# Optimization experiments

Hardware: AMD Instinct MI355X
Metric: run time of the kernel (lower is better)

Reference implementation:

```python
import jax, jax.numpy as jnp
import numpy as np

MARGIN = 0.3
NUM_CLASSES = 1000


def setup_inputs() -> dict:
    key = jax.random.key(0)
    k1, k2 = jax.random.split(key)
    B, D = 8192, 256
    inputs = jax.random.normal(k1, (B, D), dtype=jnp.float32)
    targets = jax.random.randint(k2, (B,), 0, NUM_CLASSES, dtype=jnp.int64)
    return {"inputs": inputs, "targets": targets}


def reference(inputs, targets):
    # Squared Euclidean pairwise distances: ||x_i||^2 + ||x_j||^2 - 2 x_i.x_j
    sq = jnp.sum(inputs * inputs, axis=1)                      # [B]
    dist = sq[:, None] + sq[None, :] - 2.0 * (inputs @ inputs.T)  # [B, B]

    # Hard mining: per-row max over positives (same label, incl. self),
    # min over negatives, exactly as the torch per-row masked max/min loop.
    pos_mask = targets[:, None] == targets[None, :]            # [B, B] bool
    neg_inf = jnp.float32(-jnp.inf)
    pos_inf = jnp.float32(jnp.inf)
    dist_ap = jnp.max(jnp.where(pos_mask, dist, neg_inf), axis=1)  # [B]
    dist_an = jnp.min(jnp.where(pos_mask, pos_inf, dist), axis=1)  # [B]

    # MarginRankingLoss(margin)(dist_an, dist_ap, y=1) = mean relu(ap - an + m)
    loss = jnp.mean(jax.nn.relu(dist_ap - dist_an + MARGIN))
    prec = jnp.mean((dist_an > dist_ap).astype(jnp.float32))
    return (loss, prec)
```

## Files before the change

### kernel.cpp

```cpp
#include <hip/hip_runtime.h>
#include <hip/hip_bf16.h>

#define B_N 8192
#define D_K 256
#define MARGIN 0.3f

typedef float f32x4 __attribute__((ext_vector_type(4)));
typedef short s16x8 __attribute__((ext_vector_type(8)));

__device__ __forceinline__ unsigned fkey(float f) {
    unsigned u = __float_as_uint(f);
    return (u & 0x80000000u) ? ~u : (u | 0x80000000u);
}
__device__ __forceinline__ float kval(unsigned k) {
    return (k & 0x80000000u) ? __uint_as_float(k ^ 0x80000000u)
                             : __uint_as_float(~k);
}

__device__ __forceinline__ void load_lds16(const unsigned short* g,
                                           unsigned short* l) {
    __builtin_amdgcn_global_load_lds(
        (const __attribute__((address_space(1))) unsigned int*)g,
        (__attribute__((address_space(3))) unsigned int*)l, 16, 0, 0);
}

__global__ __launch_bounds__(256) void prep_kernel(const float* __restrict__ X,
        float* __restrict__ sq, unsigned* __restrict__ apk,
        unsigned* __restrict__ ank, unsigned short* __restrict__ Xp,
        float* __restrict__ acc2) {
    int row  = (blockIdx.x << 2) + (threadIdx.x >> 6);
    int lane = threadIdx.x & 63;
    const float4 v = reinterpret_cast<const float4*>(X + (size_t)row * D_K)[lane];

    float xs[4] = {v.x, v.y, v.z, v.w};
    ushort4 hv;
    unsigned short* hp = &hv.x;
    float s = 0.f;
    #pragma unroll
    for (int i = 0; i < 4; ++i) {
        __hip_bfloat16 h = __float2bfloat16(xs[i]);
        hp[i] = *reinterpret_cast<unsigned short*>(&h);
        float hf = __bfloat162float(h);
        s = fmaf(hf, hf, s);
    }
    *reinterpret_cast<ushort4*>(Xp + (size_t)row * D_K + lane * 4) = hv;

    #pragma unroll
    for (int o = 32; o > 0; o >>= 1) s += __shfl_down(s, o, 64);
    if (lane == 0) {
        sq[row]  = s;
        apk[row] = 0u;
        ank[row] = 0xFFFFFFFFu;
    }
    if (blockIdx.x == 0 && threadIdx.x == 0) {
        acc2[0] = 0.f; acc2[1] = 0.f;
        reinterpret_cast<unsigned*>(acc2)[2] = 0u;
    }
}

#define BM 128
#define BN 128

__global__ __launch_bounds__(256, 2) void dist_kernel(
        const unsigned short* __restrict__ Xp,
        const int* __restrict__ tgt, const float* __restrict__ sq,
        unsigned* __restrict__ apk, unsigned* __restrict__ ank) {
    __shared__ unsigned short Atile[2][128 * 64];
    __shared__ unsigned short Btile[2][128 * 64];

    const int t    = threadIdx.x;
    const int lane = t & 63;
    const int wave = t >> 6;
    const int wrow = (wave >> 1) * 64;
    const int wcol = (wave & 1) * 64;
    const int fr   = lane & 15;
    const int quad = lane >> 4;
    const float INF = __int_as_float(0x7f800000);

    int tt = blockIdx.x;
    int bx = (int)((sqrtf(8.f * (float)tt + 1.f) - 1.f) * 0.5f);
    while ((bx + 1) * (bx + 2) / 2 <= tt) ++bx;
    while (bx * (bx + 1) / 2 > tt) --bx;
    int by = tt - bx * (bx + 1) / 2;
    const int bm = by * BM;
    const int bn = bx * BN;

    int ct[4]; float csq[4];
    #pragma unroll
    for (int ni = 0; ni < 4; ++ni) {
        int c = bn + wcol + ni * 16 + fr;
        ct[ni] = tgt[c]; csq[ni] = sq[c];
    }
    int rt[16]; float rsq[16];
    #pragma unroll
    for (int mi = 0; mi < 4; ++mi)
        #pragma unroll
        for (int reg = 0; reg < 4; ++reg) {
            int r = bm + wrow + mi * 16 + quad * 4 + reg;
            rt[mi * 4 + reg]  = tgt[r];
            rsq[mi * 4 + reg] = sq[r];
        }

    const unsigned short* ag[4];
    const unsigned short* bg[4];
    int loff[4];
    #pragma unroll
    for (int j = 0; j < 4; ++j) {
        int g = wave * 64 + j * 256 + lane;
        int r = g >> 3, s0 = g & 7;
        int u = s0 ^ (r & 7);
        ag[j] = Xp + (size_t)(bm + r) * D_K + u * 8;
        bg[j] = Xp + (size_t)(bn + r) * D_K + u * 8;
        loff[j] = g * 8;
    }

    int aoff[4][2], boff[4][2];
    #pragma unroll
    for (int mi = 0; mi < 4; ++mi)
        #pragma unroll
        for (int h = 0; h < 2; ++h) {
            int s = (h * 4 + quad) ^ (fr & 7);
            aoff[mi][h] = (wrow + mi * 16 + fr) * 64 + s * 8;
            boff[mi][h] = (wcol + mi * 16 + fr) * 64 + s * 8;
        }

    #pragma unroll
    for (int j = 0; j < 4; ++j) {
        load_lds16(ag[j], &Atile[0][loff[j]]);
        load_lds16(bg[j], &Btile[0][loff[j]]);
    }

    f32x4 acc[4][4];
    #pragma unroll
    for (int i = 0; i < 4; ++i)
        #pragma unroll
        for (int j = 0; j < 4; ++j) acc[i][j] = (f32x4){0.f, 0.f, 0.f, 0.f};

    __syncthreads();

    #pragma unroll
    for (int win = 0; win < 4; ++win) {
        const int cur = win & 1;
        if (win < 3) {
            const int wo = (win + 1) * 64;
            #pragma unroll
            for (int j = 0; j < 4; ++j) {
                load_lds16(ag[j] + wo, &Atile[cur ^ 1][loff[j]]);
                load_lds16(bg[j] + wo, &Btile[cur ^ 1][loff[j]]);
            }
        }
        s16x8 a[4][2], b[4][2];
        #pragma unroll
        for (int mi = 0; mi < 4; ++mi)
            #pragma unroll
            for (int h = 0; h < 2; ++h) {
                a[mi][h] = *reinterpret_cast<const s16x8*>(&Atile[cur][aoff[mi][h]]);
                b[mi][h] = *reinterpret_cast<const s16x8*>(&Btile[cur][boff[mi][h]]);
            }
        __builtin_amdgcn_s_setprio(1);
        #pragma unroll
        for (int mi = 0; mi < 4; ++mi)
            #pragma unroll
            for (int ni = 0; ni < 4; ++ni) {
                acc[mi][ni] = __builtin_amdgcn_mfma_f32_16x16x32_bf16(
                    a[mi][0], b[ni][0], acc[mi][ni], 0, 0, 0);
                acc[mi][ni] = __builtin_amdgcn_mfma_f32_16x16x32_bf16(
                    a[mi][1], b[ni][1], acc[mi][ni], 0, 0, 0);
            }
        __builtin_amdgcn_s_setprio(0);
        if (win < 3) __syncthreads();
    }

    float cap[4], can[4];
    #pragma unroll
    for (int ni = 0; ni < 4; ++ni) { cap[ni] = -INF; can[ni] = INF; }

    #pragma unroll
    for (int mi = 0; mi < 4; ++mi) {
        #pragma unroll
        for (int reg = 0; reg < 4; ++reg) {
            int rl = wrow + mi * 16 + quad * 4 + reg;
            int   rti  = rt[mi * 4 + reg];
            float rsqi = rsq[mi * 4 + reg];
            float rap = -INF, ran = INF;
            #pragma unroll
            for (int ni = 0; ni < 4; ++ni) {
                float d = rsqi + csq[ni] - 2.f * acc[mi][ni][reg];
                bool pos = (rti == ct[ni]);
                if (pos) { rap = fmaxf(rap, d); cap[ni] = fmaxf(cap[ni], d); }
                else     { ran = fminf(ran, d); can[ni] = fminf(can[ni], d); }
            }
            #pragma unroll
            for (int o = 1; o < 16; o <<= 1) {
                rap = fmaxf(rap, __shfl_xor(rap, o, 64));
                ran = fminf(ran, __shfl_xor(ran, o, 64));
            }
            if (fr == 0) {
                atomicMax(&apk[bm + rl], fkey(rap));
                atomicMin(&ank[bm + rl], fkey(ran));
            }
        }
    }
    #pragma unroll
    for (int ni = 0; ni < 4; ++ni) {
        #pragma unroll
        for (int o = 16; o < 64; o <<= 1) {
            cap[ni] = fmaxf(cap[ni], __shfl_xor(cap[ni], o, 64));
            can[ni] = fminf(can[ni], __shfl_xor(can[ni], o, 64));
        }
    }
    if (lane < 16) {
        #pragma unroll
        for (int ni = 0; ni < 4; ++ni) {
            int c = bn + wcol + ni * 16 + lane;
            atomicMax(&apk[c], fkey(cap[ni]));
            atomicMin(&ank[c], fkey(can[ni]));
        }
    }
}

__global__ __launch_bounds__(256) void final_kernel(const unsigned* __restrict__ apk,
        const unsigned* __restrict__ ank, float* __restrict__ acc2,
        float* __restrict__ out) {
    __shared__ float s_sum[4], s_cnt[4];
    int i = blockIdx.x * 256 + threadIdx.x;
    float ap = kval(apk[i]);
    float an = kval(ank[i]);
    float v  = ap - an + MARGIN;
    float sum = v > 0.f ? v : 0.f;
    float cnt = an > ap ? 1.f : 0.f;
    #pragma unroll
    for (int o = 32; o > 0; o >>= 1) {
        sum += __shfl_down(sum, o, 64);
        cnt += __shfl_down(cnt, o, 64);
    }
    int wave = threadIdx.x >> 6, lane = threadIdx.x & 63;
    if (lane == 0) { s_sum[wave] = sum; s_cnt[wave] = cnt; }
    __syncthreads();
    if (threadIdx.x == 0) {
        float ts = 0.f, tc = 0.f;
        #pragma unroll
        for (int w = 0; w < 4; ++w) { ts += s_sum[w]; tc += s_cnt[w]; }
        atomicAdd(&acc2[0], ts);
        atomicAdd(&acc2[1], tc);
        __threadfence();
        unsigned ticket = atomicAdd(reinterpret_cast<unsigned*>(acc2) + 2, 1u);
        if (ticket == gridDim.x - 1) {
            float fs = atomicAdd(&acc2[0], 0.f);
            float fc = atomicAdd(&acc2[1], 0.f);
            out[0] = fs / (float)B_N;
            out[1] = fc / (float)B_N;
        }
    }
}

extern "C" void kernel_launch(void* const* d_in, const int* in_sizes, int n_in,
                              void* d_out, int out_size, void* d_ws, size_t ws_size,
                              hipStream_t stream) {
    const float* X   = (const float*)d_in[0];
    const int*   tgt = (const int*)d_in[1];

    char* ws = (char*)d_ws;
    float*          sq   = (float*)ws;
    unsigned*       apk  = (unsigned*)(ws + 32768);
    unsigned*       ank  = (unsigned*)(ws + 65536);
    float*          acc2 = (float*)(ws + 98304);
    unsigned short* Xp   = (unsigned short*)(ws + 131072);

    float* out = (float*)d_out;

    prep_kernel<<<B_N / 4, 256, 0, stream>>>(X, sq, apk, ank, Xp, acc2);
    dist_kernel<<<(64 * 65) / 2, 256, 0, stream>>>(Xp, tgt, sq, apk, ank);
    final_kernel<<<B_N / 256, 256, 0, stream>>>(apk, ank, acc2, out);
}
```

Baseline: 126.6 us.

## Enlarge distance tiles to 256x256 with 512-thread blocks and streamed B fragments

Doubles the symmetric distance tile to 256x256 using 8 waves per block, each computing a 64x128 sub-tile, so fewer tiles and less redundant global-to-LDS traffic per output. B fragments are now loaded from LDS inside the ni loop rather than all preloaded. The row/column label and norm loads are deferred until after the GEMM, and the window loop is kept rolled to reduce register pressure. LDS per block doubles to 128KB and each thread holds 128 accumulator floats, which may cut occupancy to one block per CU. The larger tiles also leave a grid of only 528 blocks, which risks poor load balance across CUs.

```diff
diff --git a/kernel.cpp b/kernel.cpp
--- a/kernel.cpp
+++ b/kernel.cpp
@@ -58,21 +58,23 @@
     }
 }
 
-#define BM 128
-#define BN 128
-
-__global__ __launch_bounds__(256, 2) void dist_kernel(
+#define BM 256
+#define BN 256
+#define NPAN (B_N / BM)
+#define NTILE (NPAN * (NPAN + 1) / 2)
+
+__global__ __launch_bounds__(512, 2) void dist_kernel(
         const unsigned short* __restrict__ Xp,
         const int* __restrict__ tgt, const float* __restrict__ sq,
         unsigned* __restrict__ apk, unsigned* __restrict__ ank) {
-    __shared__ unsigned short Atile[2][128 * 64];
-    __shared__ unsigned short Btile[2][128 * 64];
+    __shared__ unsigned short Atile[2][BM * 64];
+    __shared__ unsigned short Btile[2][BN * 64];
 
     const int t    = threadIdx.x;
     const int lane = t & 63;
     const int wave = t >> 6;
     const int wrow = (wave >> 1) * 64;
-    const int wcol = (wave & 1) * 64;
+    const int wcol = (wave & 1) * 128;
     const int fr   = lane & 15;
     const int quad = lane >> 4;
     const float INF = __int_as_float(0x7f800000);
@@ -85,28 +87,12 @@
     const int bm = by * BM;
     const int bn = bx * BN;
 
-    int ct[4]; float csq[4];
-    #pragma unroll
-    for (int ni = 0; ni < 4; ++ni) {
-        int c = bn + wcol + ni * 16 + fr;
-        ct[ni] = tgt[c]; csq[ni] = sq[c];
-    }
-    int rt[16]; float rsq[16];
-    #pragma unroll
-    for (int mi = 0; mi < 4; ++mi)
-        #pragma unroll
-        for (int reg = 0; reg < 4; ++reg) {
-            int r = bm + wrow + mi * 16 + quad * 4 + reg;
-            rt[mi * 4 + reg]  = tgt[r];
-            rsq[mi * 4 + reg] = sq[r];
-        }
-
     const unsigned short* ag[4];
     const unsigned short* bg[4];
     int loff[4];
     #pragma unroll
     for (int j = 0; j < 4; ++j) {
-        int g = wave * 64 + j * 256 + lane;
+        int g = j * 512 + t;
         int r = g >> 3, s0 = g & 7;
         int u = s0 ^ (r & 7);
         ag[j] = Xp + (size_t)(bm + r) * D_K + u * 8;
@@ -114,15 +100,11 @@
         loff[j] = g * 8;
     }
 
-    int aoff[4][2], boff[4][2];
-    #pragma unroll
-    for (int mi = 0; mi < 4; ++mi)
-        #pragma unroll
-        for (int h = 0; h < 2; ++h) {
-            int s = (h * 4 + quad) ^ (fr & 7);
-            aoff[mi][h] = (wrow + mi * 16 + fr) * 64 + s * 8;
-            boff[mi][h] = (wcol + mi * 16 + fr) * 64 + s * 8;
-        }
+    f32x4 acc[4][8];
+    #pragma unroll
+    for (int i = 0; i < 4; ++i)
+        #pragma unroll
+        for (int j = 0; j < 8; ++j) acc[i][j] = (f32x4){0.f, 0.f, 0.f, 0.f};
 
     #pragma unroll
     for (int j = 0; j < 4; ++j) {
@@ -130,61 +112,67 @@
         load_lds16(bg[j], &Btile[0][loff[j]]);
     }
 
-    f32x4 acc[4][4];
-    #pragma unroll
-    for (int i = 0; i < 4; ++i)
-        #pragma unroll
-        for (int j = 0; j < 4; ++j) acc[i][j] = (f32x4){0.f, 0.f, 0.f, 0.f};
-
-    __syncthreads();
-
-    #pragma unroll
+    #pragma unroll 1
     for (int win = 0; win < 4; ++win) {
-        const int cur = win & 1;
+        __syncthreads();
         if (win < 3) {
             const int wo = (win + 1) * 64;
+            const int nb = (win + 1) & 1;
             #pragma unroll
             for (int j = 0; j < 4; ++j) {
-                load_lds16(ag[j] + wo, &Atile[cur ^ 1][loff[j]]);
-                load_lds16(bg[j] + wo, &Btile[cur ^ 1][loff[j]]);
-            }
-        }
-        s16x8 a[4][2], b[4][2];
+                load_lds16(ag[j] + wo, &Atile[nb][loff[j]]);
+                load_lds16(bg[j] + wo, &Btile[nb][loff[j]]);
+            }
+        }
+        const int cur = win & 1;
+        s16x8 a[4][2];
         #pragma unroll
         for (int mi = 0; mi < 4; ++mi)
             #pragma unroll
             for (int h = 0; h < 2; ++h) {
-                a[mi][h] = *reinterpret_cast<const s16x8*>(&Atile[cur][aoff[mi][h]]);
-                b[mi][h] = *reinterpret_cast<const s16x8*>(&Btile[cur][boff[mi][h]]);
+                int s = (h * 4 + quad) ^ (fr & 7);
+                a[mi][h] = *reinterpret_cast<const s16x8*>(
+                    &Atile[cur][(wrow + mi * 16 + fr) * 64 + s * 8]);
             }
         __builtin_amdgcn_s_setprio(1);
         #pragma unroll
-        for (int mi = 0; mi < 4; ++mi)
-            #pragma unroll
-            for (int ni = 0; ni < 4; ++ni) {
+        for (int ni = 0; ni < 8; ++ni) {
+            int rb = (wcol + ni * 16 + fr) * 64;
+            int s0b = quad ^ (fr & 7);
+            int s1b = (4 + quad) ^ (fr & 7);
+            s16x8 b0 = *reinterpret_cast<const s16x8*>(&Btile[cur][rb + s0b * 8]);
+            s16x8 b1 = *reinterpret_cast<const s16x8*>(&Btile[cur][rb + s1b * 8]);
+            #pragma unroll
+            for (int mi = 0; mi < 4; ++mi) {
                 acc[mi][ni] = __builtin_amdgcn_mfma_f32_16x16x32_bf16(
-                    a[mi][0], b[ni][0], acc[mi][ni], 0, 0, 0);
+                    a[mi][0], b0, acc[mi][ni], 0, 0, 0);
                 acc[mi][ni] = __builtin_amdgcn_mfma_f32_16x16x32_bf16(
-                    a[mi][1], b[ni][1], acc[mi][ni], 0, 0, 0);
-            }
+                    a[mi][1], b1, acc[mi][ni], 0, 0, 0);
+            }
+        }
         __builtin_amdgcn_s_setprio(0);
-        if (win < 3) __syncthreads();
-    }
-
-    float cap[4], can[4];
-    #pragma unroll
-    for (int ni = 0; ni < 4; ++ni) { cap[ni] = -INF; can[ni] = INF; }
+    }
+
+    int ct[8]; float csq[8];
+    #pragma unroll
+    for (int ni = 0; ni < 8; ++ni) {
+        int c = bn + wcol + ni * 16 + fr;
+        ct[ni] = tgt[c]; csq[ni] = sq[c];
+    }
+    float cap[8], can[8];
+    #pragma unroll
+    for (int ni = 0; ni < 8; ++ni) { cap[ni] = -INF; can[ni] = INF; }
 
     #pragma unroll
     for (int mi = 0; mi < 4; ++mi) {
         #pragma unroll
         for (int reg = 0; reg < 4; ++reg) {
             int rl = wrow + mi * 16 + quad * 4 + reg;
-            int   rti  = rt[mi * 4 + reg];
-            float rsqi = rsq[mi * 4 + reg];
+            int rti = tgt[bm + rl];
+            float rsqi = sq[bm + rl];
             float rap = -INF, ran = INF;
             #pragma unroll
-            for (int ni = 0; ni < 4; ++ni) {
+            for (int ni = 0; ni < 8; ++ni) {
                 float d = rsqi + csq[ni] - 2.f * acc[mi][ni][reg];
                 bool pos = (rti == ct[ni]);
                 if (pos) { rap = fmaxf(rap, d); cap[ni] = fmaxf(cap[ni], d); }
@@ -202,7 +190,7 @@
         }
     }
     #pragma unroll
-    for (int ni = 0; ni < 4; ++ni) {
+    for (int ni = 0; ni < 8; ++ni) {
         #pragma unroll
         for (int o = 16; o < 64; o <<= 1) {
             cap[ni] = fmaxf(cap[ni], __shfl_xor(cap[ni], o, 64));
@@ -211,7 +199,7 @@
     }
     if (lane < 16) {
         #pragma unroll
-        for (int ni = 0; ni < 4; ++ni) {
+        for (int ni = 0; ni < 8; ++ni) {
             int c = bn + wcol + ni * 16 + lane;
             atomicMax(&apk[c], fkey(cap[ni]));
             atomicMin(&ank[c], fkey(can[ni]));
@@ -270,6 +258,6 @@
     float* out = (float*)d_out;
 
     prep_kernel<<<B_N / 4, 256, 0, stream>>>(X, sq, apk, ank, Xp, acc2);
-    dist_kernel<<<(64 * 65) / 2, 256, 0, stream>>>(Xp, tgt, sq, apk, ank);
+    dist_kernel<<<NTILE, 512, 0, stream>>>(Xp, tgt, sq, apk, ank);
     final_kernel<<<B_N / 256, 256, 0, stream>>>(apk, ank, acc2, out);
 }
```

Measured after the change: 127.7 us. No clear change (+0.9%).
